# Kernel tuning notes

Hardware: AMD Instinct MI355X
Metric: run time of the kernel (lower is better)

## Reference

```python
import jax, jax.numpy as jnp
import numpy as np

NUM_HEADS = 8
HEAD_DIM = 16
NEG_SLOPE = 0.2


def setup_inputs() -> dict:
    key = jax.random.key(0)
    k1, k2, k3, k4, k5 = jax.random.split(key, 5)
    N, E, D_IN, D_OUT = 100000, 1600000, 128, 128
    x = jax.random.normal(k1, (N, D_IN), dtype=jnp.float32)
    edge_indices = jax.random.randint(k2, (2, E), 0, N, dtype=jnp.int64)
    W = jax.random.normal(k3, (D_OUT, D_IN), dtype=jnp.float32) * (1.0 / np.sqrt(D_IN))
    src_attn = jax.random.normal(k4, (1, NUM_HEADS, HEAD_DIM), dtype=jnp.float32) * (1.0 / np.sqrt(HEAD_DIM))
    dst_attn = jax.random.normal(k5, (1, NUM_HEADS, HEAD_DIM), dtype=jnp.float32) * (1.0 / np.sqrt(HEAD_DIM))
    return {"x": x, "edge_indices": edge_indices, "W": W, "src_attn": src_attn, "dst_attn": dst_attn}


def reference(x, edge_indices, W, src_attn, dst_attn):
    N = x.shape[0]
    # add self loops (i, i) for every node
    loops = jnp.arange(N, dtype=edge_indices.dtype)
    ei = jnp.concatenate([edge_indices, jnp.stack([loops, loops])], axis=1)  # [2, E+N]
    row, col = ei[0], ei[1]

    # linear projection + head split: [N, H, hd]
    h = (x @ W.T).reshape(N, NUM_HEADS, HEAD_DIM)

    # per-node attention logits, gathered per edge: [E', H]
    s = jnp.sum(h * src_attn, axis=-1)  # [N, H]
    d = jnp.sum(h * dst_attn, axis=-1)  # [N, H]
    e = jax.nn.leaky_relu(s[row] + d[col], negative_slope=NEG_SLOPE)  # [E', H]

    # sparse softmax over each row's neighborhood (dim=1 of the sparse matrix)
    m = jax.ops.segment_max(e, row, num_segments=N)  # [N, H]
    e = jnp.exp(e - m[row])
    z = jax.ops.segment_sum(e, row, num_segments=N)  # [N, H]
    a = e / z[row]  # [E', H]

    # per-head SpMM: out[row] += a * h[col]
    out = jax.ops.segment_sum(a[:, :, None] * h[col], row, num_segments=N)  # [N, H, hd]
    return out.reshape(N, NUM_HEADS * HEAD_DIM)
```

## Files before the change

kernel.cpp:

```cpp
#include <hip/hip_runtime.h>
#include <hip/hip_bf16.h>
#include <math.h>

#define NEG_SLOPE 0.2f

typedef __attribute__((ext_vector_type(8))) short short8v;
typedef __attribute__((ext_vector_type(4))) float f32x4;

__global__ __launch_bounds__(256) void gat_prep(
    const float* __restrict__ W, const float* __restrict__ srcA,
    const float* __restrict__ dstA, ushort* __restrict__ wbf,
    int* __restrict__ count8, int cn,
    unsigned int* __restrict__ state, int* __restrict__ ticket)
{
  int gtid = blockIdx.x * 256 + threadIdx.x;
  for (int i = gtid; i < cn; i += gridDim.x * 256)
    count8[i] = 0;
  if (gtid < 256) state[gtid] = 0;
  if (gtid == 0) *ticket = 0;

  if (gtid >= 36 * 64) return;
  int frag = gtid >> 6, lane = gtid & 63;
  int nt = frag >> 2, ks = frag & 3;
  int kbase = ks * 32 + (lane >> 4) * 8;
  ushort v[8];
  if (nt < 8) {
    int r = nt * 16 + (lane & 15);
#pragma unroll
    for (int j = 0; j < 8; ++j)
      v[j] = __bfloat16_as_ushort(__float2bfloat16(W[(size_t)r * 128 + kbase + j]));
  } else {
    int n = lane & 15;
    int hd = n & 7;
    const float* av = (n < 8) ? srcA : dstA;
#pragma unroll
    for (int j = 0; j < 8; ++j) {
      float acc = 0.f;
      int k = kbase + j;
      for (int d = 0; d < 16; ++d)
        acc += W[(size_t)(hd * 16 + d) * 128 + k] * av[hd * 16 + d];
      v[j] = __bfloat16_as_ushort(__float2bfloat16(acc));
    }
  }
  ushort* dst = wbf + ((size_t)frag * 64 + lane) * 8;
#pragma unroll
  for (int j = 0; j < 8; ++j) dst[j] = v[j];
}

__global__ __launch_bounds__(256, 2) void gat_gemm_hist(
    const float* __restrict__ x, const ushort* __restrict__ wbf,
    ushort* __restrict__ hb, float* __restrict__ s, float* __restrict__ dv,
    int N, int nchunks, int G1,
    const int* __restrict__ ei, int E, int* __restrict__ count8,
    int* __restrict__ rank, int userank, int npriv)
{
  const int q = (int)blockIdx.x / 5;
  const int r5 = (int)blockIdx.x % 5;
  if (r5 == 0) {
    const int wave = threadIdx.x >> 6, lane = threadIdx.x & 63;
    const int lrow = lane & 15, lkg = lane >> 4;

    short8v b[36];
    const short8v* wv = (const short8v*)wbf;
#pragma unroll
    for (int f = 0; f < 36; ++f) b[f] = wv[(size_t)f * 64 + lane];

    for (int chunk = q; chunk < nchunks; chunk += G1) {
      const int r0 = chunk * 64 + wave * 16;
      int arow = r0 + lrow; if (arow > N - 1) arow = N - 1;
      const float* xr = x + (size_t)arow * 128 + lkg * 8;

      f32x4 acc[9];
#pragma unroll
      for (int t = 0; t < 9; ++t) acc[t] = (f32x4){0.f, 0.f, 0.f, 0.f};

#pragma unroll
      for (int ks = 0; ks < 4; ++ks) {
        float4 x0 = *(const float4*)(xr + ks * 32);
        float4 x1 = *(const float4*)(xr + ks * 32 + 4);
        short8v a;
        a[0] = (short)__bfloat16_as_ushort(__float2bfloat16(x0.x));
        a[1] = (short)__bfloat16_as_ushort(__float2bfloat16(x0.y));
        a[2] = (short)__bfloat16_as_ushort(__float2bfloat16(x0.z));
        a[3] = (short)__bfloat16_as_ushort(__float2bfloat16(x0.w));
        a[4] = (short)__bfloat16_as_ushort(__float2bfloat16(x1.x));
        a[5] = (short)__bfloat16_as_ushort(__float2bfloat16(x1.y));
        a[6] = (short)__bfloat16_as_ushort(__float2bfloat16(x1.z));
        a[7] = (short)__bfloat16_as_ushort(__float2bfloat16(x1.w));
#pragma unroll
        for (int t = 0; t < 9; ++t)
          acc[t] = __builtin_amdgcn_mfma_f32_16x16x32_bf16(a, b[t * 4 + ks], acc[t], 0, 0, 0);
      }

      const int rbase = r0 + lkg * 4;
#pragma unroll
      for (int t = 0; t < 8; ++t) {
#pragma unroll
        for (int r = 0; r < 4; ++r) {
          int row = rbase + r;
          if (row < N)
            hb[(size_t)row * 128 + t * 16 + lrow] =
                __bfloat16_as_ushort(__float2bfloat16(acc[t][r]));
        }
      }
#pragma unroll
      for (int r = 0; r < 4; ++r) {
        int row = rbase + r;
        if (row < N) {
          if (lrow < 8) s[(size_t)row * 8 + lrow] = acc[8][r];
          else          dv[(size_t)row * 8 + (lrow - 8)] = acc[8][r];
        }
      }
    }
  } else {
    __shared__ int sh64;
    if (threadIdx.x == 0) sh64 = 1;
    __syncthreads();
    if (ei[2 * threadIdx.x + 1] != 0) sh64 = 0;
    __syncthreads();
    const int is64 = sh64;
    const int k = (int)(blockIdx.x & (unsigned)(npriv - 1));
    int* cnt = count8 + (size_t)k * N;

    const int hb_id = q * 4 + (r5 - 1);
    const int nhb = 4 * G1;
    int i = hb_id * 256 + threadIdx.x;
    const int stride = nhb * 256;
    for (; i < E; i += stride) {
      int r = is64 ? ei[2 * i] : ei[i];
      int old = atomicAdd(&cnt[r], 1);
      if (userank) rank[i] = old | (k << 28);
    }
  }
}

template<int NPRIV>
__global__ __launch_bounds__(256) void gat_scan(
    const int* __restrict__ count8, int N, int nb,
    unsigned int* __restrict__ state, int* __restrict__ ticket,
    int* __restrict__ offsets, int* __restrict__ suboff,
    int* __restrict__ selfpos, int total, int userank)
{
  __shared__ int sbid;
  __shared__ int sm[256];
  __shared__ int sprefix;
  if (threadIdx.x == 0) sbid = atomicAdd(ticket, 1);
  __syncthreads();
  const int bid = sbid;
  const int base = bid * 1024 + threadIdx.x * 4;

  int c[4][NPRIV];
  int v[4];
  int tsum = 0;
#pragma unroll
  for (int j = 0; j < 4; ++j) {
    int idx = base + j;
    int cs = 0;
#pragma unroll
    for (int k = 0; k < NPRIV; ++k) {
      int cv = (idx < N) ? count8[(size_t)k * N + idx] : 0;
      c[j][k] = cv; cs += cv;
    }
    v[j] = (idx < N) ? cs + 1 : 0;
    tsum += v[j];
  }

  sm[threadIdx.x] = tsum;
  __syncthreads();
  int acc = tsum;
  for (int off = 1; off < 256; off <<= 1) {
    int other = (threadIdx.x >= off) ? sm[threadIdx.x - off] : 0;
    __syncthreads();
    acc += other;
    sm[threadIdx.x] = acc;
    __syncthreads();
  }
  const int blocktotal = sm[255];

  if (threadIdx.x == 0)
    __hip_atomic_store(&state[bid], (1u << 30) | (unsigned)blocktotal,
                       __ATOMIC_RELEASE, __HIP_MEMORY_SCOPE_AGENT);
  if (threadIdx.x < 64) {
    const int lane = threadIdx.x;
    int ex = 0;
    int j = bid - 1;
    while (j >= 0) {
      int idx = j - lane;
      unsigned d = (idx >= 0)
          ? __hip_atomic_load(&state[idx], __ATOMIC_ACQUIRE, __HIP_MEMORY_SCOPE_AGENT)
          : (2u << 30);
      unsigned st = d >> 30;
      unsigned long long m2 = __ballot(st == 2u);
      unsigned long long m0 = __ballot(st == 0u);
      int f2 = m2 ? ((int)__ffsll((long long)m2) - 1) : 64;
      int f0 = m0 ? ((int)__ffsll((long long)m0) - 1) : 64;
      if (f0 < f2) continue;
      int take = (lane < f2 || (lane == f2 && f2 < 64)) ? (int)(d & 0x3FFFFFFFu) : 0;
#pragma unroll
      for (int off = 1; off < 64; off <<= 1) take += __shfl_xor(take, off, 64);
      ex += take;
      if (f2 < 64) break;
      j -= 64;
    }
    if (lane == 0) {
      __hip_atomic_store(&state[bid], (2u << 30) | (unsigned)(ex + blocktotal),
                         __ATOMIC_RELEASE, __HIP_MEMORY_SCOPE_AGENT);
      sprefix = ex;
    }
  }
  __syncthreads();

  int e = sprefix + acc - tsum;
#pragma unroll
  for (int j = 0; j < 4; ++j) {
    int idx = base + j;
    if (idx < N) {
      offsets[idx] = e;
      int run = e;
#pragma unroll
      for (int k = 0; k < NPRIV; ++k) { suboff[(size_t)k * N + idx] = run; run += c[j][k]; }
      selfpos[idx] = userank ? run : e;
      e += v[j];
    }
  }
  if (bid == nb - 1 && threadIdx.x == 255) offsets[N] = total;
}

__global__ __launch_bounds__(256) void gat_scatter_rank(
    const int* __restrict__ ei, int E, int N,
    const int* __restrict__ suboff, const int* __restrict__ selfpos,
    const int* __restrict__ rank, int* __restrict__ scol)
{
  __shared__ int sh64;
  if (threadIdx.x == 0) sh64 = 1;
  __syncthreads();
  if (ei[2 * threadIdx.x + 1] != 0) sh64 = 0;
  __syncthreads();
  const int is64 = sh64;

  int i = blockIdx.x * 256 + threadIdx.x;
  const int stride = gridDim.x * 256;
  const int total = E + N;
  for (; i < total; i += stride) {
    int pos, c;
    if (i < E) {
      int r;
      if (is64) { r = ei[2 * i]; c = ei[2 * (E + i)]; }
      else      { r = ei[i];     c = ei[E + i]; }
      int pr = rank[i];
      int k = (int)(((unsigned)pr) >> 28);
      pos = suboff[(size_t)k * N + r] + (pr & 0x0FFFFFFF);
    } else {
      int r = i - E; c = r;
      pos = selfpos[r];
    }
    scol[pos] = c;
  }
}

__global__ __launch_bounds__(256) void gat_scatter(
    const int* __restrict__ ei, int E, int N,
    int* __restrict__ cursor, int* __restrict__ scol)
{
  __shared__ int sh64;
  if (threadIdx.x == 0) sh64 = 1;
  __syncthreads();
  if (ei[2 * threadIdx.x + 1] != 0) sh64 = 0;
  __syncthreads();
  const int is64 = sh64;

  int i = blockIdx.x * 256 + threadIdx.x;
  const int stride = gridDim.x * 256;
  const int total = E + N;
  for (; i < total; i += stride) {
    int r, c;
    if (i < E) {
      if (is64) { r = ei[2 * i]; c = ei[2 * (E + i)]; }
      else      { r = ei[i];     c = ei[E + i]; }
    } else {
      r = i - E; c = r;
    }
    int pos = atomicAdd(&cursor[r], 1);
    scol[pos] = c;
  }
}

__global__ __launch_bounds__(256) void gat_agg(
    const uint* __restrict__ hb, const float* __restrict__ s, const float* __restrict__ dv,
    const int* __restrict__ offsets, const int* __restrict__ scol,
    float* __restrict__ out, int N)
{
  int wid = (int)((blockIdx.x * 256 + threadIdx.x) >> 6);
  int lane = threadIdx.x & 63;
  if (wid >= N) return;
  const int g = lane >> 4;
  const int t = lane & 15;
  const int head = t >> 1;
  const int beg = __builtin_amdgcn_readfirstlane(offsets[wid]);
  const int end = __builtin_amdgcn_readfirstlane(offsets[wid + 1]);
  const float sl = s[wid * 8 + head];

  const char* hbp = (const char*)hb;
  const char* dvp = (const char*)dv;
  const uint hoff = (uint)t * 16u;
  const uint doff = (uint)head * 4u;

  float z = 0.f;
  float a0 = 0, a1 = 0, a2 = 0, a3 = 0, a4 = 0, a5 = 0, a6 = 0, a7 = 0;

  const int nq = (end - beg + 3) >> 2;
  const int lasti = end - 1;

  int iA = beg + g;       iA = iA < end ? iA : lasti;
  int iB = beg + 4 + g;   iB = iB < end ? iB : lasti;
  int iC = beg + 8 + g;   iC = iC < end ? iC : lasti;
  int cB = scol[iB];
  int cC = scol[iC];
  int cA = scol[iA];
  float dlA = *(const float*)(dvp + ((uint)cA * 32u + doff));
  uint4 huA = *(const uint4*)(hbp + ((uint)cA * 256u + hoff));
  float dlB = *(const float*)(dvp + ((uint)cB * 32u + doff));
  uint4 huB = *(const uint4*)(hbp + ((uint)cB * 256u + hoff));

  for (int j = 0; j < nq; ++j) {
    int iD = beg + 4 * (j + 3) + g; iD = iD < end ? iD : lasti;
    int cD = scol[iD];
    float dlC = *(const float*)(dvp + ((uint)cC * 32u + doff));
    uint4 huC = *(const uint4*)(hbp + ((uint)cC * 256u + hoff));

    float e = sl + dlA;
    e = fmaxf(e, NEG_SLOPE * e);
    float w = (beg + 4 * j + g < end) ? __expf(e) : 0.f;
    z += w;
    a0 = fmaf(w, __uint_as_float(huA.x << 16), a0);
    a1 = fmaf(w, __uint_as_float(huA.x & 0xFFFF0000u), a1);
    a2 = fmaf(w, __uint_as_float(huA.y << 16), a2);
    a3 = fmaf(w, __uint_as_float(huA.y & 0xFFFF0000u), a3);
    a4 = fmaf(w, __uint_as_float(huA.z << 16), a4);
    a5 = fmaf(w, __uint_as_float(huA.z & 0xFFFF0000u), a5);
    a6 = fmaf(w, __uint_as_float(huA.w << 16), a6);
    a7 = fmaf(w, __uint_as_float(huA.w & 0xFFFF0000u), a7);

    dlA = dlB; huA = huB;
    dlB = dlC; huB = huC;
    cC = cD;
  }

  a0 += __shfl_xor(a0, 16, 64); a0 += __shfl_xor(a0, 32, 64);
  a1 += __shfl_xor(a1, 16, 64); a1 += __shfl_xor(a1, 32, 64);
  a2 += __shfl_xor(a2, 16, 64); a2 += __shfl_xor(a2, 32, 64);
  a3 += __shfl_xor(a3, 16, 64); a3 += __shfl_xor(a3, 32, 64);
  a4 += __shfl_xor(a4, 16, 64); a4 += __shfl_xor(a4, 32, 64);
  a5 += __shfl_xor(a5, 16, 64); a5 += __shfl_xor(a5, 32, 64);
  a6 += __shfl_xor(a6, 16, 64); a6 += __shfl_xor(a6, 32, 64);
  a7 += __shfl_xor(a7, 16, 64); a7 += __shfl_xor(a7, 32, 64);
  z  += __shfl_xor(z, 16, 64);  z  += __shfl_xor(z, 32, 64);

  float inv = 1.f / z;
  if (lane < 16) {
    float4* op = (float4*)(out + (size_t)wid * 128 + t * 8);
    op[0] = make_float4(a0 * inv, a1 * inv, a2 * inv, a3 * inv);
    op[1] = make_float4(a4 * inv, a5 * inv, a6 * inv, a7 * inv);
  }
}

extern "C" void kernel_launch(void* const* d_in, const int* in_sizes, int n_in,
                              void* d_out, int out_size, void* d_ws, size_t ws_size,
                              hipStream_t stream) {
  const float* x    = (const float*)d_in[0];
  const int*   ei   = (const int*)d_in[1];
  const float* W    = (const float*)d_in[2];
  const float* srcA = (const float*)d_in[3];
  const float* dstA = (const float*)d_in[4];
  float* out = (float*)d_out;
  const int N = in_sizes[0] / 128;
  const int E = in_sizes[1] / 2;

  auto need = [&](int npriv, int userank) -> size_t {
    size_t b = (size_t)N * 128 * 2;
    b += (size_t)N * 8 * 4 * 2;
    b += 36864;
    b += (size_t)npriv * N * 4;
    b += (size_t)(N + 1) * 4;
    b += (size_t)npriv * N * 4;
    b += (size_t)N * 4;
    b += 256 * 4 + 16;
    b += (size_t)(E + N) * 4;
    if (userank) b += (size_t)E * 4;
    return b;
  };
  int npriv = 8, userank = 1;
  if (need(8, 1) > ws_size) { npriv = 1; userank = 1; }
  if (need(1, 1) > ws_size) { npriv = 1; userank = 0; }

  ushort* hbuf = (ushort*)d_ws;
  float* s  = (float*)(hbuf + (size_t)N * 128);
  float* dv = s + (size_t)N * 8;
  ushort* wbf = (ushort*)(dv + (size_t)N * 8);
  int* count8  = (int*)((char*)wbf + 36864);
  int* offsets = count8 + (size_t)npriv * N;
  int* suboff  = offsets + (N + 1);
  int* selfpos = suboff + (size_t)npriv * N;
  unsigned int* state = (unsigned int*)(selfpos + N);
  int* ticket  = (int*)(state + 256);
  int* scol    = ticket + 4;
  int* rank    = scol + (E + N);

  const int nchunks = (N + 63) / 64;
  const int G1 = 512;
  const int nb = (N + 1023) / 1024;

  gat_prep<<<2048, 256, 0, stream>>>(W, srcA, dstA, wbf, count8, npriv * N, state, ticket);
  gat_gemm_hist<<<5 * G1, 256, 0, stream>>>(x, wbf, hbuf, s, dv, N, nchunks, G1,
                                            ei, E, count8, rank, userank, npriv);
  if (npriv == 8)
    gat_scan<8><<<nb, 256, 0, stream>>>(count8, N, nb, state, ticket, offsets,
                                        suboff, selfpos, E + N, userank);
  else
    gat_scan<1><<<nb, 256, 0, stream>>>(count8, N, nb, state, ticket, offsets,
                                        suboff, selfpos, E + N, userank);
  if (userank)
    gat_scatter_rank<<<2048, 256, 0, stream>>>(ei, E, N, suboff, selfpos, rank, scol);
  else
    gat_scatter<<<2048, 256, 0, stream>>>(ei, E, N, selfpos, scol);
  gat_agg<<<(N + 3) / 4, 256, 0, stream>>>((const uint*)hbuf, s, dv, offsets, scol, out, N);
}
```

Measured before the change: 207.8 us.

## Rebalance GEMM/histogram block split and process edges in vectorized pairs

```diff
diff --git a/kernel.cpp b/kernel.cpp
--- a/kernel.cpp
+++ b/kernel.cpp
@@ -50,13 +50,14 @@
 __global__ __launch_bounds__(256, 2) void gat_gemm_hist(
     const float* __restrict__ x, const ushort* __restrict__ wbf,
     ushort* __restrict__ hb, float* __restrict__ s, float* __restrict__ dv,
-    int N, int nchunks, int G1,
+    int N, int nchunks, int NG, int NH,
     const int* __restrict__ ei, int E, int* __restrict__ count8,
-    int* __restrict__ rank, int userank, int npriv)
+    int* __restrict__ rank, int userank)
 {
   const int q = (int)blockIdx.x / 5;
   const int r5 = (int)blockIdx.x % 5;
-  if (r5 == 0) {
+  if (r5 < 3) {
+    const int gemmId = q * 3 + r5;
     const int wave = threadIdx.x >> 6, lane = threadIdx.x & 63;
     const int lrow = lane & 15, lkg = lane >> 4;
 
@@ -65,7 +66,7 @@
 #pragma unroll
     for (int f = 0; f < 36; ++f) b[f] = wv[(size_t)f * 64 + lane];
 
-    for (int chunk = q; chunk < nchunks; chunk += G1) {
+    for (int chunk = gemmId; chunk < nchunks; chunk += NG) {
       const int r0 = chunk * 64 + wave * 16;
       int arow = r0 + lrow; if (arow > N - 1) arow = N - 1;
       const float* xr = x + (size_t)arow * 128 + lkg * 8;
@@ -119,17 +120,28 @@
     if (ei[2 * threadIdx.x + 1] != 0) sh64 = 0;
     __syncthreads();
     const int is64 = sh64;
-    const int k = (int)(blockIdx.x & (unsigned)(npriv - 1));
+    const int k = (int)(blockIdx.x & 7u);
     int* cnt = count8 + (size_t)k * N;
 
-    const int hb_id = q * 4 + (r5 - 1);
-    const int nhb = 4 * G1;
-    int i = hb_id * 256 + threadIdx.x;
-    const int stride = nhb * 256;
-    for (; i < E; i += stride) {
-      int r = is64 ? ei[2 * i] : ei[i];
-      int old = atomicAdd(&cnt[r], 1);
-      if (userank) rank[i] = old | (k << 28);
+    const int histId = q * 2 + (r5 - 3);
+    const int npairs = (E + 1) >> 1;
+    const int pstride = NH * 256;
+    for (int p = histId * 256 + threadIdx.x; p < npairs; p += pstride) {
+      int r0, r1;
+      const int i1ok = (2 * p + 1) < E;
+      if (is64) {
+        int4 rr = *(const int4*)(ei + 4 * (size_t)p);
+        r0 = rr.x; r1 = rr.z;
+      } else {
+        int2 rr = ((const int2*)ei)[p];
+        r0 = rr.x; r1 = rr.y;
+      }
+      int old0 = atomicAdd(&cnt[r0], 1);
+      int old1 = i1ok ? atomicAdd(&cnt[r1], 1) : 0;
+      if (userank) {
+        if (i1ok) ((int2*)rank)[p] = make_int2(old0 | (k << 28), old1 | (k << 28));
+        else      rank[2 * p] = old0 | (k << 28);
+      }
     }
   }
 }
@@ -238,24 +250,35 @@
   __syncthreads();
   const int is64 = sh64;
 
-  int i = blockIdx.x * 256 + threadIdx.x;
+  const int gid = blockIdx.x * 256 + threadIdx.x;
   const int stride = gridDim.x * 256;
-  const int total = E + N;
-  for (; i < total; i += stride) {
-    int pos, c;
-    if (i < E) {
-      int r;
-      if (is64) { r = ei[2 * i]; c = ei[2 * (E + i)]; }
-      else      { r = ei[i];     c = ei[E + i]; }
-      int pr = rank[i];
-      int k = (int)(((unsigned)pr) >> 28);
-      pos = suboff[(size_t)k * N + r] + (pr & 0x0FFFFFFF);
+  const int npairs = (E + 1) >> 1;
+  for (int p = gid; p < npairs; p += stride) {
+    int r0, r1, c0, c1;
+    const int i1ok = (2 * p + 1) < E;
+    if (is64) {
+      int4 rr = *(const int4*)(ei + 4 * (size_t)p);
+      int2 ca = *(const int2*)(ei + 2 * (size_t)E + 4 * (size_t)p);
+      int2 cb = *(const int2*)(ei + 2 * (size_t)E + 4 * (size_t)p + 2);
+      r0 = rr.x; r1 = rr.z; c0 = ca.x; c1 = cb.x;
     } else {
-      int r = i - E; c = r;
-      pos = selfpos[r];
-    }
-    scol[pos] = c;
-  }
+      int2 rr = ((const int2*)ei)[p];
+      r0 = rr.x; r1 = rr.y;
+      c0 = ei[E + 2 * p];
+      c1 = i1ok ? ei[E + 2 * p + 1] : 0;
+    }
+    int2 pr = ((const int2*)rank)[p];
+    int k0 = (int)(((unsigned)pr.x) >> 28);
+    int pos0 = suboff[(size_t)k0 * N + r0] + (pr.x & 0x0FFFFFFF);
+    scol[pos0] = c0;
+    if (i1ok) {
+      int k1 = (int)(((unsigned)pr.y) >> 28);
+      int pos1 = suboff[(size_t)k1 * N + r1] + (pr.y & 0x0FFFFFFF);
+      scol[pos1] = c1;
+    }
+  }
+  for (int j = gid; j < N; j += stride)
+    scol[selfpos[j]] = j;
 }
 
 __global__ __launch_bounds__(256) void gat_scatter(
@@ -386,7 +409,7 @@
     b += (size_t)N * 4;
     b += 256 * 4 + 16;
     b += (size_t)(E + N) * 4;
-    if (userank) b += (size_t)E * 4;
+    if (userank) b += (size_t)(E + 1) * 4;
     return b;
   };
   int npriv = 8, userank = 1;
@@ -407,12 +430,12 @@
   int* rank    = scol + (E + N);
 
   const int nchunks = (N + 63) / 64;
-  const int G1 = 512;
+  const int NG = 1536, NH = 1024;
   const int nb = (N + 1023) / 1024;
 
   gat_prep<<<2048, 256, 0, stream>>>(W, srcA, dstA, wbf, count8, npriv * N, state, ticket);
-  gat_gemm_hist<<<5 * G1, 256, 0, stream>>>(x, wbf, hbuf, s, dv, N, nchunks, G1,
-                                            ei, E, count8, rank, userank, npriv);
+  gat_gemm_hist<<<2560, 256, 0, stream>>>(x, wbf, hbuf, s, dv, N, nchunks, NG, NH,
+                                          ei, E, count8, rank, userank);
   if (npriv == 8)
     gat_scan<8><<<nb, 256, 0, stream>>>(count8, N, nb, state, ticket, offsets,
                                         suboff, selfpos, E + N, userank);
```

After: 202.2 us. 1.03x faster.
